# Kernel optimization log

Hardware: AMD Instinct MI355X
Metric: run time of the kernel (lower is better)

## Reference

```python
import jax, jax.numpy as jnp
import numpy as np

D_MODEL = 768
N_LAYER = 4
VOCAB = 50257
D_STATE = 16
D_CONV = 4
D_INNER = 2 * D_MODEL
DT_RANK = 48
B, L = 1, 2048


def setup_inputs() -> dict:
    key = jax.random.key(0)
    ks = jax.random.split(key, 12)
    n = lambda k, shape, s=0.02: jax.random.normal(k, shape, dtype=jnp.float32) * s
    return {
        "idx": jax.random.randint(ks[0], (B, L), 0, VOCAB, dtype=jnp.int32),
        "targets": jax.random.randint(ks[1], (B, L), 0, VOCAB, dtype=jnp.int32),
        "embedding": n(ks[2], (VOCAB, D_MODEL)),
        "norm_w": jnp.ones((N_LAYER, D_MODEL), jnp.float32),
        "in_proj_w": n(ks[3], (N_LAYER, 2 * D_INNER, D_MODEL)),
        "conv_w": n(ks[4], (N_LAYER, D_INNER, D_CONV), 0.1),
        "conv_b": jnp.zeros((N_LAYER, D_INNER), jnp.float32),
        "x_proj_w": n(ks[5], (N_LAYER, DT_RANK + 2 * D_STATE, D_INNER)),
        "dt_proj_w": n(ks[6], (N_LAYER, D_INNER, DT_RANK), 0.1),
        # bias so softplus(dt) lands in ~[0.01, 0.1] as in the official init
        "dt_proj_b": jax.random.uniform(ks[7], (N_LAYER, D_INNER), jnp.float32, -4.6, -2.3),
        # A_log = log(1..d_state), the standard S4D-real init
        "A_log": jnp.log(jnp.broadcast_to(jnp.arange(1, D_STATE + 1, dtype=jnp.float32), (N_LAYER, D_INNER, D_STATE))),
        "D_param": jnp.ones((N_LAYER, D_INNER), jnp.float32),
        "out_proj_w": n(ks[8], (N_LAYER, D_MODEL, D_INNER)),
        "norm_f_w": jnp.ones((D_MODEL,), jnp.float32),
    }


def rmsnorm(x, w, eps=1e-5):
    return x * jax.lax.rsqrt(jnp.mean(x * x, -1, keepdims=True) + eps) * w


def causal_conv1d(x, w, b):
    # x: (B,L,d_inner); w: (d_inner, K) depthwise causal conv
    K = w.shape[-1]
    Lx = x.shape[1]
    xp = jnp.pad(x, ((0, 0), (K - 1, 0), (0, 0)))
    y = b
    for k in range(K):
        y = y + xp[:, k:k + Lx, :] * w[:, k]
    return y


def selective_scan(x, dt, A, Bm, Cm, Dp):
    # x, dt: (B,L,d_inner); A: (d_inner,d_state); Bm, Cm: (B,L,d_state)
    bsz, _, d_in = x.shape

    def step(h, inp):
        x_t, dt_t, B_t, C_t = inp  # (B,d_in),(B,d_in),(B,s),(B,s)
        h = jnp.exp(dt_t[:, :, None] * A) * h + (dt_t * x_t)[:, :, None] * B_t[:, None, :]
        return h, jnp.einsum('bds,bs->bd', h, C_t)

    h0 = jnp.zeros((bsz, d_in, A.shape[-1]), x.dtype)
    _, ys = jax.lax.scan(step, h0, (x.swapaxes(0, 1), dt.swapaxes(0, 1), Bm.swapaxes(0, 1), Cm.swapaxes(0, 1)))
    return ys.swapaxes(0, 1) + x * Dp


def mamba_block(x, in_w, cw, cb, xpw, dtw, dtb, a_log, dp, ow):
    xz = x @ in_w.T  # (B,L,2*d_inner)
    xi, z = jnp.split(xz, 2, axis=-1)
    xi = jax.nn.silu(causal_conv1d(xi, cw, cb))
    xdbl = xi @ xpw.T  # (B,L,dt_rank+2*d_state)
    dt = xdbl[..., :DT_RANK]
    Bm = xdbl[..., DT_RANK:DT_RANK + D_STATE]
    Cm = xdbl[..., DT_RANK + D_STATE:]
    dt = jax.nn.softplus(dt @ dtw.T + dtb)
    A = -jnp.exp(a_log)
    y = selective_scan(xi, dt, A, Bm, Cm, dp)
    y = y * jax.nn.silu(z)
    return y @ ow.T


def reference(idx, targets, embedding, norm_w, in_proj_w, conv_w, conv_b, x_proj_w,
              dt_proj_w, dt_proj_b, A_log, D_param, out_proj_w, norm_f_w):
    x = embedding[idx]  # (B,L,D)
    for l in range(N_LAYER):
        x = x + mamba_block(rmsnorm(x, norm_w[l]), in_proj_w[l], conv_w[l], conv_b[l],
                            x_proj_w[l], dt_proj_w[l], dt_proj_b[l], A_log[l],
                            D_param[l], out_proj_w[l])
    x = rmsnorm(x, norm_f_w)
    logits = x @ embedding.T  # tied lm head, (B,L,V)
    # cross_entropy with ignore_index=-1
    logp = jax.nn.log_softmax(logits, axis=-1)
    mask = (targets >= 0).astype(logits.dtype)
    tgt = jnp.clip(targets, 0, VOCAB - 1)
    nll = -jnp.take_along_axis(logp, tgt[..., None], axis=-1)[..., 0]
    loss = jnp.sum(nll * mask) / jnp.maximum(jnp.sum(mask), 1.0)
    return (logits, loss)
```

## Files before the change

### kernel.cpp

```cpp
#include <hip/hip_runtime.h>
#include <stdint.h>


#define D_MODEL 768
#define N_LAYER 4
#define VOCAB 50257
#define D_STATE 16
#define D_INNER 1536
#define DT_RANK 48
#define LSEQ 2048
#define TCHUNK 64
#define NCHUNK 32

#define EMB_E 39321600L
#define W1E 2359296L
#define W2E 196608L
#define W3E 98304L
#define W4E 1179648L
#define PERL (W1E + W2E + W3E + W4E)
#define TOTCVT (EMB_E + 4 * PERL)

typedef unsigned short u16;
typedef __attribute__((ext_vector_type(8))) short short8;
typedef __attribute__((ext_vector_type(4))) float f32x4;

__device__ __forceinline__ u16 f2bf(float f) {
  unsigned int x = __float_as_uint(f);
  x += 0x7fffu + ((x >> 16) & 1u);
  return (u16)(x >> 16);
}
__device__ __forceinline__ float bf2f(u16 v) {
  return __uint_as_float(((unsigned int)v) << 16);
}
__device__ __forceinline__ void gl16(const void* g, void* l) {
  __builtin_amdgcn_global_load_lds((const __attribute__((address_space(1))) void*)g,
                                   (__attribute__((address_space(3))) void*)l, 16, 0, 0);
}

#define PIPELINE(NT)                                                          \
  STAGE(0, 0);                                                                \
  STAGE(32, 1);                                                               \
  {                                                                           \
    int cur = 0;                                                              \
    for (int t = 0; t < (NT); t++) {                                          \
      if (t + 1 < (NT)) { asm volatile("s_waitcnt vmcnt(4)" ::: "memory"); }  \
      else              { asm volatile("s_waitcnt vmcnt(0)" ::: "memory"); }  \
      asm volatile("s_barrier" ::: "memory");                                 \
      short8 af[4], bfr[4];                                                   \
      _Pragma("unroll")                                                       \
      for (int i = 0; i < 4; i++)                                             \
        af[i] = *(const short8*)(&lA[cur][(wm + i * 16 + fr) * 32 + kh]);     \
      _Pragma("unroll")                                                       \
      for (int j = 0; j < 4; j++)                                             \
        bfr[j] = *(const short8*)(&lB[cur][(wn + j * 16 + fr) * 32 + kh]);    \
      asm volatile("s_waitcnt lgkmcnt(0)" ::: "memory");                      \
      asm volatile("s_barrier" ::: "memory");                                 \
      if (t + 2 < (NT)) STAGE((t + 2) * 32, cur);                             \
      _Pragma("unroll")                                                       \
      for (int i = 0; i < 4; i++)                                             \
        _Pragma("unroll")                                                     \
        for (int j = 0; j < 4; j++)                                           \
          acc[i][j] = __builtin_amdgcn_mfma_f32_16x16x32_bf16(af[i], bfr[j],  \
                                                              acc[i][j], 0, 0, 0); \
      cur ^= 1;                                                               \
    }                                                                         \
  }

__global__ void k_convert_all(const float* __restrict__ emb, const float* __restrict__ in_w,
                              const float* __restrict__ xp_w, const float* __restrict__ dt_w,
                              const float* __restrict__ out_w, u16* __restrict__ dst) {
  long i = (long)blockIdx.x * 256 + threadIdx.x;
  float v;
  if (i < EMB_E) {
    long n = i / D_MODEL, k = i % D_MODEL;
    v = (n < VOCAB) ? emb[n * D_MODEL + k] : 0.0f;
  } else {
    long j = i - EMB_E;
    int l = (int)(j / PERL);
    long m = j % PERL;
    if (m < W1E) {
      v = in_w[(long)l * W1E + m];
    } else if (m < W1E + W2E) {
      long mm = m - W1E;
      long n = mm / D_INNER, k = mm % D_INNER;
      v = (n < 80) ? xp_w[(long)l * 80 * D_INNER + n * D_INNER + k] : 0.0f;
    } else if (m < W1E + W2E + W3E) {
      long mm = m - (W1E + W2E);
      long n = mm / 64, k = mm % 64;
      v = (k < DT_RANK) ? dt_w[(long)l * D_INNER * DT_RANK + n * DT_RANK + k] : 0.0f;
    } else {
      long mm = m - (W1E + W2E + W3E);
      v = out_w[(long)l * W4E + mm];
    }
  }
  dst[i] = f2bf(v);
}

__global__ void k_embed_rms(const int* __restrict__ idx, const float* __restrict__ emb,
                            const float* __restrict__ w, float* __restrict__ x,
                            u16* __restrict__ xnb) {
  int t = blockIdx.x, tid = threadIdx.x;
  __shared__ float red[256];
  const float* src = emb + (long)idx[t] * D_MODEL;
  float g[3];
  float s = 0.0f;
#pragma unroll
  for (int q = 0; q < 3; q++) {
    g[q] = src[tid + q * 256];
    s += g[q] * g[q];
  }
  red[tid] = s; __syncthreads();
  for (int o = 128; o > 0; o >>= 1) { if (tid < o) red[tid] += red[tid + o]; __syncthreads(); }
  float scale = rsqrtf(red[0] / (float)D_MODEL + 1e-5f);
#pragma unroll
  for (int q = 0; q < 3; q++) {
    int c = tid + q * 256;
    x[(long)t * D_MODEL + c] = g[q];
    xnb[(long)t * D_MODEL + c] = f2bf(g[q] * scale * w[c]);
  }
}

__global__ void k_rms_red(const float* __restrict__ part, const float* __restrict__ w,
                          float* __restrict__ x, u16* __restrict__ xnb) {
  int t = blockIdx.x, tid = threadIdx.x;
  __shared__ float red[256];
  float g[3];
  float s = 0.0f;
#pragma unroll
  for (int q = 0; q < 3; q++) {
    int c = tid + q * 256;
    long off = (long)t * D_MODEL + c;
    float v = x[off];
#pragma unroll
    for (int p = 0; p < 4; p++) v += part[(size_t)p * LSEQ * D_MODEL + off];
    g[q] = v;
    s += v * v;
  }
  red[tid] = s; __syncthreads();
  for (int o = 128; o > 0; o >>= 1) { if (tid < o) red[tid] += red[tid + o]; __syncthreads(); }
  float scale = rsqrtf(red[0] / (float)D_MODEL + 1e-5f);
#pragma unroll
  for (int q = 0; q < 3; q++) {
    int c = tid + q * 256;
    x[(long)t * D_MODEL + c] = g[q];
    xnb[(long)t * D_MODEL + c] = f2bf(g[q] * scale * w[c]);
  }
}

template<int EPI>
__global__ __launch_bounds__(256) void k_gemm2(
    const u16* __restrict__ A, const u16* __restrict__ W, void* __restrict__ Cv,
    const float* __restrict__ bias, int N, int K, int lda, int ldb, int ldc) {
  __shared__ u16 lA[2][128 * 32];
  __shared__ u16 lB[2][128 * 32];
  const int gx = gridDim.x, gy = gridDim.y;
  int id = blockIdx.x + gx * blockIdx.y;
  int q8 = (gx * gy) >> 3;
  int v = (id & 7) * q8 + (id >> 3);
  const int bx = v / gy, by = v % gy;
  const int brow = by * 128, bcol = bx * 128;
  const int tid = threadIdx.x, wid = tid >> 6, lane = tid & 63;
  const int wm = (wid >> 1) * 64, wn = (wid & 1) * 64;
  const int fr = lane & 15, fq = lane >> 4, kh = fq * 8;
  const int srow = tid >> 2, scol = (tid & 3) * 8;
  const u16* ga0 = A + (size_t)(brow + srow) * lda + scol;
  const u16* ga1 = A + (size_t)(brow + srow + 64) * lda + scol;
  const u16* gb0 = W + (size_t)(bcol + srow) * ldb + scol;
  const u16* gb1 = W + (size_t)(bcol + srow + 64) * ldb + scol;
  const int lo = srow * 32 + scol;

  f32x4 acc[4][4];
#pragma unroll
  for (int i = 0; i < 4; i++)
#pragma unroll
    for (int j = 0; j < 4; j++)
#pragma unroll
      for (int r = 0; r < 4; r++) acc[i][j][r] = 0.0f;

  auto STAGE = [&](int k0, int b) {
    gl16(ga0 + k0, &lA[b][lo]);
    gl16(ga1 + k0, &lA[b][lo + 2048]);
    gl16(gb0 + k0, &lB[b][lo]);
    gl16(gb1 + k0, &lB[b][lo + 2048]);
  };

  PIPELINE(K / 32);

#pragma unroll
  for (int i = 0; i < 4; i++)
#pragma unroll
    for (int j = 0; j < 4; j++) {
      int col = bcol + wn + j * 16 + fr;
      if (col < N) {
#pragma unroll
        for (int r = 0; r < 4; r++) {
          int row = brow + wm + i * 16 + fq * 4 + r;
          float val = acc[i][j][r];
          if (EPI == 1) {
            val += bias[col];
            val = (val > 20.0f) ? val : log1pf(__expf(val));
            ((float*)Cv)[(size_t)row * ldc + col] = val;
          } else {
            ((u16*)Cv)[(size_t)row * ldc + col] = f2bf(val);
          }
        }
      }
    }
}

__global__ __launch_bounds__(256) void k_gemm_part(
    const u16* __restrict__ A, const u16* __restrict__ W, float* __restrict__ Cp,
    int N, int Ks, int lda, int ldb, int ldc) {
  __shared__ u16 lA[2][128 * 32];
  __shared__ u16 lB[2][128 * 32];
  const int gx = gridDim.x, gy = gridDim.y;
  int id = blockIdx.x + gx * blockIdx.y;
  int q8 = (gx * gy) >> 3;
  int v = (id & 7) * q8 + (id >> 3);
  const int bx = v / gy, by = v % gy;
  const int brow = by * 128, bcol = bx * 128;
  const int koff = blockIdx.z * Ks;
  const int tid = threadIdx.x, wid = tid >> 6, lane = tid & 63;
  const int wm = (wid >> 1) * 64, wn = (wid & 1) * 64;
  const int fr = lane & 15, fq = lane >> 4, kh = fq * 8;
  const int srow = tid >> 2, scol = (tid & 3) * 8;
  const u16* ga0 = A + (size_t)(brow + srow) * lda + koff + scol;
  const u16* ga1 = A + (size_t)(brow + srow + 64) * lda + koff + scol;
  const u16* gb0 = W + (size_t)(bcol + srow) * ldb + koff + scol;
  const u16* gb1 = W + (size_t)(bcol + srow + 64) * ldb + koff + scol;
  const int lo = srow * 32 + scol;

  f32x4 acc[4][4];
#pragma unroll
  for (int i = 0; i < 4; i++)
#pragma unroll
    for (int j = 0; j < 4; j++)
#pragma unroll
      for (int r = 0; r < 4; r++) acc[i][j][r] = 0.0f;

  auto STAGE = [&](int k0, int b) {
    gl16(ga0 + k0, &lA[b][lo]);
    gl16(ga1 + k0, &lA[b][lo + 2048]);
    gl16(gb0 + k0, &lB[b][lo]);
    gl16(gb1 + k0, &lB[b][lo + 2048]);
  };

  PIPELINE(Ks / 32);

  float* Cz = Cp + (size_t)blockIdx.z * LSEQ * ldc;
#pragma unroll
  for (int i = 0; i < 4; i++)
#pragma unroll
    for (int j = 0; j < 4; j++) {
      int col = bcol + wn + j * 16 + fr;
      if (col < N) {
#pragma unroll
        for (int r = 0; r < 4; r++) {
          int row = brow + wm + i * 16 + fq * 4 + r;
          Cz[(size_t)row * ldc + col] = acc[i][j][r];
        }
      }
    }
}

__global__ __launch_bounds__(256) void k_gemm_logits(
    const u16* __restrict__ A, const u16* __restrict__ W, float* __restrict__ C,
    float* __restrict__ part) {
  __shared__ u16 lA[2][128 * 32];
  __shared__ u16 lB[2][128 * 32];
  const int b = blockIdx.x;
  const int xcd = b & 7, slot = b >> 3;
  const int ct = xcd * 50 + (slot >> 4), rt = slot & 15;
  const int brow = rt * 128, bcol = ct * 128;
  const int tid = threadIdx.x, wid = tid >> 6, lane = tid & 63;
  const int wm = (wid >> 1) * 64, wn = (wid & 1) * 64;
  const int fr = lane & 15, fq = lane >> 4, kh = fq * 8;
  const int srow = tid >> 2, scol = (tid & 3) * 8;
  const u16* ga0 = A + (size_t)(brow + srow) * D_MODEL + scol;
  const u16* ga1 = A + (size_t)(brow + srow + 64) * D_MODEL + scol;
  const u16* gb0 = W + (size_t)(bcol + srow) * D_MODEL + scol;
  const u16* gb1 = W + (size_t)(bcol + srow + 64) * D_MODEL + scol;
  const int lo = srow * 32 + scol;

  f32x4 acc[4][4];
#pragma unroll
  for (int i = 0; i < 4; i++)
#pragma unroll
    for (int j = 0; j < 4; j++)
#pragma unroll
      for (int r = 0; r < 4; r++) acc[i][j][r] = 0.0f;

  auto STAGE = [&](int k0, int bb) {
    gl16(ga0 + k0, &lA[bb][lo]);
    gl16(ga1 + k0, &lA[bb][lo + 2048]);
    gl16(gb0 + k0, &lB[bb][lo]);
    gl16(gb1 + k0, &lB[bb][lo + 2048]);
  };

  PIPELINE(D_MODEL / 32);

  float rs[16];
#pragma unroll
  for (int q = 0; q < 16; q++) rs[q] = 0.0f;
#pragma unroll
  for (int i = 0; i < 4; i++)
#pragma unroll
    for (int j = 0; j < 4; j++) {
      int col = bcol + wn + j * 16 + fr;
      if (col < VOCAB) {
#pragma unroll
        for (int r = 0; r < 4; r++) {
          int row = brow + wm + i * 16 + fq * 4 + r;
          float val = acc[i][j][r];
          C[(size_t)row * VOCAB + col] = val;
          rs[i * 4 + r] += __expf(val - 20.0f);
        }
      }
    }
#pragma unroll
  for (int q = 0; q < 16; q++) {
    float s = rs[q];
    s += __shfl_xor(s, 1); s += __shfl_xor(s, 2);
    s += __shfl_xor(s, 4); s += __shfl_xor(s, 8);
    rs[q] = s;
  }
  if (fr == 0) {
    int pc = ct * 2 + (wn >> 6);
#pragma unroll
    for (int i = 0; i < 4; i++)
#pragma unroll
      for (int r = 0; r < 4; r++) {
        int row = brow + wm + i * 16 + fq * 4 + r;
        part[(size_t)pc * LSEQ + row] = rs[i * 4 + r];
      }
  }
}

__global__ void k_conv_silu(const u16* __restrict__ xzb, const float* __restrict__ cw,
                            const float* __restrict__ cb, u16* __restrict__ xib) {
  int i = blockIdx.x * 256 + threadIdx.x;
  int t = i / (D_INNER / 8), d8 = (i % (D_INNER / 8)) * 8;
  float acc[8];
#pragma unroll
  for (int q = 0; q < 8; q++) acc[q] = cb[d8 + q];
#pragma unroll
  for (int k = 0; k < 4; k++) {
    int tt = t - 3 + k;
    if (tt >= 0) {
      short8 v = *(const short8*)(xzb + (long)tt * (2 * D_INNER) + d8);
#pragma unroll
      for (int q = 0; q < 8; q++) acc[q] += bf2f((u16)v[q]) * cw[(d8 + q) * 4 + k];
    }
  }
  short8 o;
#pragma unroll
  for (int q = 0; q < 8; q++) {
    float s = acc[q] / (1.0f + __expf(-acc[q]));
    o[q] = (short)f2bf(s);
  }
  *(short8*)(xib + (long)t * D_INNER + d8) = o;
}

__global__ void k_red_xd(const float* __restrict__ pxp, float* __restrict__ xdbl,
                         u16* __restrict__ dtp) {
  int i = blockIdx.x * 256 + threadIdx.x;
  int t = i >> 7, k = i & 127;
  if (k < 80) {
    float s = 0.0f;
#pragma unroll
    for (int p = 0; p < 8; p++) s += pxp[(size_t)p * LSEQ * 80 + (long)t * 80 + k];
    xdbl[(long)t * 80 + k] = s;
    if (k < DT_RANK) dtp[(long)t * 64 + k] = f2bf(s);
    else if (k < 64) dtp[(long)t * 64 + k] = 0;
  }
}

__global__ void k_scanA(const float* __restrict__ dt, const u16* __restrict__ xi,
                        const float* __restrict__ xdbl, const float* __restrict__ a_log,
                        float* __restrict__ aprod, float* __restrict__ hend) {
  int d = blockIdx.x * 256 + threadIdx.x;
  int c = blockIdx.y;
  float A[16], ap[16], h[16];
#pragma unroll
  for (int s = 0; s < 16; s++) { A[s] = -__expf(a_log[d * 16 + s]); ap[s] = 1.0f; h[s] = 0.0f; }
  int t0 = c * TCHUNK;
  for (int t = t0; t < t0 + TCHUNK; t++) {
    float dtv = dt[(long)t * D_INNER + d], xv = bf2f(xi[(long)t * D_INNER + d]);
    float dx = dtv * xv;
    const float* Bp = xdbl + (long)t * 80 + DT_RANK;
#pragma unroll
    for (int s = 0; s < 16; s++) {
      float a = __expf(dtv * A[s]);
      h[s] = a * h[s] + dx * Bp[s];
      ap[s] *= a;
    }
  }
  long base = ((long)c * D_INNER + d) * 16;
#pragma unroll
  for (int s = 0; s < 16; s++) { aprod[base + s] = ap[s]; hend[base + s] = h[s]; }
}

__global__ void k_scanB(const float* __restrict__ aprod, const float* __restrict__ hend,
                        float* __restrict__ hinit) {
  int i = blockIdx.x * 256 + threadIdx.x;
  float h = 0.0f;
  for (int c = 0; c < NCHUNK; c++) {
    long idx = (long)c * D_INNER * 16 + i;
    hinit[idx] = h;
    h = aprod[idx] * h + hend[idx];
  }
}

__global__ void k_scanC(const float* __restrict__ dt, const u16* __restrict__ xi,
                        const float* __restrict__ xdbl, const float* __restrict__ a_log,
                        const float* __restrict__ hinit, const float* __restrict__ Dp,
                        const u16* __restrict__ xzb, u16* __restrict__ yb) {
  int d = blockIdx.x * 256 + threadIdx.x;
  int c = blockIdx.y;
  float A[16], h[16];
  long hb = (long)c * D_INNER * 16 + (long)d * 16;
#pragma unroll
  for (int s = 0; s < 16; s++) { A[s] = -__expf(a_log[d * 16 + s]); h[s] = hinit[hb + s]; }
  float Dv = Dp[d];
  int t0 = c * TCHUNK;
  for (int t = t0; t < t0 + TCHUNK; t++) {
    float dtv = dt[(long)t * D_INNER + d], xv = bf2f(xi[(long)t * D_INNER + d]);
    float dx = dtv * xv;
    const float* Bp = xdbl + (long)t * 80 + DT_RANK;
    const float* Cp = Bp + D_STATE;
    float o = xv * Dv;
#pragma unroll
    for (int s = 0; s < 16; s++) {
      float a = __expf(dtv * A[s]);
      h[s] = a * h[s] + dx * Bp[s];
      o += h[s] * Cp[s];
    }
    float z = bf2f(xzb[(long)t * (2 * D_INNER) + D_INNER + d]);
    yb[(long)t * D_INNER + d] = f2bf(o * (z / (1.0f + __expf(-z))));
  }
}

__global__ void k_lse_final(const float* __restrict__ part, const float* __restrict__ logits,
                            const int* __restrict__ tgt, float* __restrict__ nll,
                            float* __restrict__ msk) {
  int t = blockIdx.x * 256 + threadIdx.x;
  float s = 0.0f;
  for (int p = 0; p < 800; p++) s += part[(size_t)p * LSEQ + t];
  float lse = 20.0f + __logf(s);
  int tg = tgt[t];
  float mk = tg >= 0 ? 1.0f : 0.0f;
  int tc = tg < 0 ? 0 : (tg > VOCAB - 1 ? VOCAB - 1 : tg);
  nll[t] = (lse - logits[(size_t)t * VOCAB + tc]) * mk;
  msk[t] = mk;
}

__global__ void k_loss(const float* __restrict__ nll, const float* __restrict__ msk,
                       float* __restrict__ out) {
  int tid = threadIdx.x;
  __shared__ float r1[256], r2[256];
  float a = 0.0f, b = 0.0f;
  for (int i = tid; i < LSEQ; i += 256) { a += nll[i]; b += msk[i]; }
  r1[tid] = a; r2[tid] = b; __syncthreads();
  for (int o = 128; o > 0; o >>= 1) {
    if (tid < o) { r1[tid] += r1[tid + o]; r2[tid] += r2[tid + o]; }
    __syncthreads();
  }
  if (tid == 0) out[0] = r1[0] / fmaxf(r2[0], 1.0f);
}

extern "C" void kernel_launch(void* const* d_in, const int* in_sizes, int n_in,
                              void* d_out, int out_size, void* d_ws, size_t ws_size,
                              hipStream_t stream) {
  const int*   idx    = (const int*)d_in[0];
  const int*   tgt    = (const int*)d_in[1];
  const float* emb    = (const float*)d_in[2];
  const float* norm_w = (const float*)d_in[3];
  const float* in_w   = (const float*)d_in[4];
  const float* conv_w = (const float*)d_in[5];
  const float* conv_b = (const float*)d_in[6];
  const float* xp_w   = (const float*)d_in[7];
  const float* dt_w   = (const float*)d_in[8];
  const float* dt_b   = (const float*)d_in[9];
  const float* a_log  = (const float*)d_in[10];
  const float* d_par  = (const float*)d_in[11];
  const float* out_w  = (const float*)d_in[12];
  const float* normf  = (const float*)d_in[13];

  float* logits = (float*)d_out;
  float* loss   = logits + (size_t)LSEQ * VOCAB;

  char* base = (char*)d_ws;
  size_t off = 0;
  auto alloc = [&](size_t bytes) -> char* {
    char* r = base + off;
    off = (off + bytes + 255) & ~(size_t)255;
    return r;
  };
  u16*   wcat = (u16*)  alloc((size_t)TOTCVT * 2);
  float* x    = (float*)alloc((size_t)LSEQ * D_MODEL * 4);
  u16*   xnb  = (u16*)  alloc((size_t)LSEQ * D_MODEL * 2);
  u16*   xzb  = (u16*)  alloc((size_t)LSEQ * 2 * D_INNER * 2);
  u16*   xib  = (u16*)  alloc((size_t)LSEQ * D_INNER * 2);
  float* xdbl = (float*)alloc((size_t)LSEQ * 80 * 4);
  u16*   dtp  = (u16*)  alloc((size_t)LSEQ * 64 * 2);
  float* dtl  = (float*)alloc((size_t)LSEQ * D_INNER * 4);
  u16*   yb   = (u16*)  alloc((size_t)LSEQ * D_INNER * 2);
  float* pxp  = (float*)alloc((size_t)8 * LSEQ * 80 * 4);
  float* pop  = (float*)alloc((size_t)4 * LSEQ * D_MODEL * 4);
  float* apr  = (float*)alloc((size_t)NCHUNK * D_INNER * 16 * 4);
  float* hen  = (float*)alloc((size_t)NCHUNK * D_INNER * 16 * 4);
  float* hin  = (float*)alloc((size_t)NCHUNK * D_INNER * 16 * 4);
  float* nll  = (float*)alloc((size_t)LSEQ * 4);
  float* msk  = (float*)alloc((size_t)LSEQ * 4);
  float* part = pop;
  (void)ws_size; (void)in_sizes; (void)n_in; (void)out_size;

  const u16* embb = wcat;

  k_convert_all<<<(unsigned)(TOTCVT / 256), 256, 0, stream>>>(emb, in_w, xp_w, dt_w, out_w, wcat);
  k_embed_rms<<<LSEQ, 256, 0, stream>>>(idx, emb, norm_w, x, xnb);

  for (int l = 0; l < N_LAYER; l++) {
    const u16* w1 = wcat + EMB_E + (long)l * PERL;
    const u16* w2 = w1 + W1E;
    const u16* w3 = w2 + W2E;
    const u16* w4 = w3 + W3E;

    k_gemm2<2><<<dim3(24, 16), 256, 0, stream>>>(
        xnb, w1, xzb, nullptr, 2 * D_INNER, D_MODEL, D_MODEL, D_MODEL, 2 * D_INNER);

    k_conv_silu<<<(LSEQ * D_INNER / 8) / 256, 256, 0, stream>>>(
        xzb, conv_w + (long)l * D_INNER * 4, conv_b + l * D_INNER, xib);

    k_gemm_part<<<dim3(1, 16, 8), 256, 0, stream>>>(
        xib, w2, pxp, 80, D_INNER / 8, D_INNER, D_INNER, 80);
    k_red_xd<<<(LSEQ * 128) / 256, 256, 0, stream>>>(pxp, xdbl, dtp);

    k_gemm2<1><<<dim3(12, 16), 256, 0, stream>>>(
        dtp, w3, dtl, dt_b + l * D_INNER, D_INNER, 64, 64, 64, D_INNER);

    const float* al = a_log + (long)l * D_INNER * D_STATE;
    k_scanA<<<dim3(D_INNER / 256, NCHUNK), 256, 0, stream>>>(dtl, xib, xdbl, al, apr, hen);
    k_scanB<<<(D_INNER * 16) / 256, 256, 0, stream>>>(apr, hen, hin);
    k_scanC<<<dim3(D_INNER / 256, NCHUNK), 256, 0, stream>>>(
        dtl, xib, xdbl, al, hin, d_par + l * D_INNER, xzb, yb);

    k_gemm_part<<<dim3(6, 16, 4), 256, 0, stream>>>(
        yb, w4, pop, D_MODEL, D_INNER / 4, D_INNER, D_INNER, D_MODEL);

    const float* wn = (l < N_LAYER - 1) ? (norm_w + (l + 1) * D_MODEL) : normf;
    k_rms_red<<<LSEQ, 256, 0, stream>>>(pop, wn, x, xnb);
  }

  k_gemm_logits<<<400 * 16, 256, 0, stream>>>(xnb, embb, logits, part);
  k_lse_final<<<LSEQ / 256, 256, 0, stream>>>(part, logits, tgt, nll, msk);
  k_loss<<<1, 256, 0, stream>>>(nll, msk, loss);
}
```

Measured before the change: 1.210 ms.

## XOR-swizzle GEMM LDS layout and enlarge logits tile to 256x128

Adds an XOR swizzle to the K-column position of global-to-LDS staging and to the matching fragment reads in all GEMM kernels, to cut LDS bank conflicts. The logits GEMM tile grows to 256 rows per block with 8x4 MFMA accumulators per wave, halving the grid and how often embedding tiles are reloaded. Its software pipeline is now written inline with explicit waitcnt, barriers and setprio. The cost is higher register pressure under launch_bounds(256,2) and fewer blocks to hide latency.

```diff
diff --git a/kernel.cpp b/kernel.cpp
--- a/kernel.cpp
+++ b/kernel.cpp
@@ -161,13 +161,16 @@
   const int brow = by * 128, bcol = bx * 128;
   const int tid = threadIdx.x, wid = tid >> 6, lane = tid & 63;
   const int wm = (wid >> 1) * 64, wn = (wid & 1) * 64;
-  const int fr = lane & 15, fq = lane >> 4, kh = fq * 8;
-  const int srow = tid >> 2, scol = (tid & 3) * 8;
+  const int fr = lane & 15, fq = lane >> 4;
+  const int kh = 8 * (fq ^ ((fr >> 1) & 3));
+  const int srow = tid >> 2;
+  const int lcol = (tid & 3) * 8;
+  const int scol = 8 * ((tid & 3) ^ ((srow >> 1) & 3));
   const u16* ga0 = A + (size_t)(brow + srow) * lda + scol;
   const u16* ga1 = A + (size_t)(brow + srow + 64) * lda + scol;
   const u16* gb0 = W + (size_t)(bcol + srow) * ldb + scol;
   const u16* gb1 = W + (size_t)(bcol + srow + 64) * ldb + scol;
-  const int lo = srow * 32 + scol;
+  const int lo = srow * 32 + lcol;
 
   f32x4 acc[4][4];
 #pragma unroll
@@ -222,13 +225,16 @@
   const int koff = blockIdx.z * Ks;
   const int tid = threadIdx.x, wid = tid >> 6, lane = tid & 63;
   const int wm = (wid >> 1) * 64, wn = (wid & 1) * 64;
-  const int fr = lane & 15, fq = lane >> 4, kh = fq * 8;
-  const int srow = tid >> 2, scol = (tid & 3) * 8;
+  const int fr = lane & 15, fq = lane >> 4;
+  const int kh = 8 * (fq ^ ((fr >> 1) & 3));
+  const int srow = tid >> 2;
+  const int lcol = (tid & 3) * 8;
+  const int scol = 8 * ((tid & 3) ^ ((srow >> 1) & 3));
   const u16* ga0 = A + (size_t)(brow + srow) * lda + koff + scol;
   const u16* ga1 = A + (size_t)(brow + srow + 64) * lda + koff + scol;
   const u16* gb0 = W + (size_t)(bcol + srow) * ldb + koff + scol;
   const u16* gb1 = W + (size_t)(bcol + srow + 64) * ldb + koff + scol;
-  const int lo = srow * 32 + scol;
+  const int lo = srow * 32 + lcol;
 
   f32x4 acc[4][4];
 #pragma unroll
@@ -263,47 +269,76 @@
     }
 }
 
-__global__ __launch_bounds__(256) void k_gemm_logits(
+__global__ __launch_bounds__(256, 2) void k_gemm_logits(
     const u16* __restrict__ A, const u16* __restrict__ W, float* __restrict__ C,
     float* __restrict__ part) {
-  __shared__ u16 lA[2][128 * 32];
+  __shared__ u16 lA[2][256 * 32];
   __shared__ u16 lB[2][128 * 32];
   const int b = blockIdx.x;
   const int xcd = b & 7, slot = b >> 3;
-  const int ct = xcd * 50 + (slot >> 4), rt = slot & 15;
-  const int brow = rt * 128, bcol = ct * 128;
+  const int ct = xcd * 50 + (slot >> 3), rt = slot & 7;
+  const int brow = rt * 256, bcol = ct * 128;
   const int tid = threadIdx.x, wid = tid >> 6, lane = tid & 63;
-  const int wm = (wid >> 1) * 64, wn = (wid & 1) * 64;
-  const int fr = lane & 15, fq = lane >> 4, kh = fq * 8;
-  const int srow = tid >> 2, scol = (tid & 3) * 8;
-  const u16* ga0 = A + (size_t)(brow + srow) * D_MODEL + scol;
-  const u16* ga1 = A + (size_t)(brow + srow + 64) * D_MODEL + scol;
-  const u16* gb0 = W + (size_t)(bcol + srow) * D_MODEL + scol;
-  const u16* gb1 = W + (size_t)(bcol + srow + 64) * D_MODEL + scol;
-  const int lo = srow * 32 + scol;
-
-  f32x4 acc[4][4];
-#pragma unroll
-  for (int i = 0; i < 4; i++)
+  const int wm = (wid >> 1) * 128, wn = (wid & 1) * 64;
+  const int fr = lane & 15, fq = lane >> 4;
+  const int kh = 8 * (fq ^ ((fr >> 1) & 3));
+  const int srow = tid >> 2;
+  const int lcol = (tid & 3) * 8;
+  const int scol = 8 * ((tid & 3) ^ ((srow >> 1) & 3));
+  const u16* ga = A + (size_t)(brow + srow) * D_MODEL + scol;
+  const u16* gb = W + (size_t)(bcol + srow) * D_MODEL + scol;
+  const int lo = srow * 32 + lcol;
+
+  f32x4 acc[8][4];
+#pragma unroll
+  for (int i = 0; i < 8; i++)
 #pragma unroll
     for (int j = 0; j < 4; j++)
 #pragma unroll
       for (int r = 0; r < 4; r++) acc[i][j][r] = 0.0f;
 
   auto STAGE = [&](int k0, int bb) {
-    gl16(ga0 + k0, &lA[bb][lo]);
-    gl16(ga1 + k0, &lA[bb][lo + 2048]);
-    gl16(gb0 + k0, &lB[bb][lo]);
-    gl16(gb1 + k0, &lB[bb][lo + 2048]);
+    gl16(ga + k0, &lA[bb][lo]);
+    gl16(ga + (size_t)64 * D_MODEL + k0, &lA[bb][lo + 2048]);
+    gl16(ga + (size_t)128 * D_MODEL + k0, &lA[bb][lo + 4096]);
+    gl16(ga + (size_t)192 * D_MODEL + k0, &lA[bb][lo + 6144]);
+    gl16(gb + k0, &lB[bb][lo]);
+    gl16(gb + (size_t)64 * D_MODEL + k0, &lB[bb][lo + 2048]);
   };
 
-  PIPELINE(D_MODEL / 32);
-
-  float rs[16];
-#pragma unroll
-  for (int q = 0; q < 16; q++) rs[q] = 0.0f;
-#pragma unroll
-  for (int i = 0; i < 4; i++)
+  STAGE(0, 0);
+  STAGE(32, 1);
+  int cur = 0;
+  const int NT = D_MODEL / 32;
+  for (int t = 0; t < NT; t++) {
+    if (t + 1 < NT) { asm volatile("s_waitcnt vmcnt(6)" ::: "memory"); }
+    else            { asm volatile("s_waitcnt vmcnt(0)" ::: "memory"); }
+    asm volatile("s_barrier" ::: "memory");
+    short8 af[8], bfr[4];
+#pragma unroll
+    for (int i = 0; i < 8; i++)
+      af[i] = *(const short8*)(&lA[cur][(wm + i * 16 + fr) * 32 + kh]);
+#pragma unroll
+    for (int j = 0; j < 4; j++)
+      bfr[j] = *(const short8*)(&lB[cur][(wn + j * 16 + fr) * 32 + kh]);
+    asm volatile("s_waitcnt lgkmcnt(0)" ::: "memory");
+    asm volatile("s_barrier" ::: "memory");
+    if (t + 2 < NT) STAGE((t + 2) * 32, cur);
+    __builtin_amdgcn_s_setprio(1);
+#pragma unroll
+    for (int i = 0; i < 8; i++)
+#pragma unroll
+      for (int j = 0; j < 4; j++)
+        acc[i][j] = __builtin_amdgcn_mfma_f32_16x16x32_bf16(af[i], bfr[j], acc[i][j], 0, 0, 0);
+    __builtin_amdgcn_s_setprio(0);
+    cur ^= 1;
+  }
+
+  float rs[32];
+#pragma unroll
+  for (int q = 0; q < 32; q++) rs[q] = 0.0f;
+#pragma unroll
+  for (int i = 0; i < 8; i++)
 #pragma unroll
     for (int j = 0; j < 4; j++) {
       int col = bcol + wn + j * 16 + fr;
@@ -318,7 +353,7 @@
       }
     }
 #pragma unroll
-  for (int q = 0; q < 16; q++) {
+  for (int q = 0; q < 32; q++) {
     float s = rs[q];
     s += __shfl_xor(s, 1); s += __shfl_xor(s, 2);
     s += __shfl_xor(s, 4); s += __shfl_xor(s, 8);
@@ -327,7 +362,7 @@
   if (fr == 0) {
     int pc = ct * 2 + (wn >> 6);
 #pragma unroll
-    for (int i = 0; i < 4; i++)
+    for (int i = 0; i < 8; i++)
 #pragma unroll
       for (int r = 0; r < 4; r++) {
         int row = brow + wm + i * 16 + fq * 4 + r;
@@ -552,7 +587,7 @@
     k_rms_red<<<LSEQ, 256, 0, stream>>>(pop, wn, x, xnb);
   }
 
-  k_gemm_logits<<<400 * 16, 256, 0, stream>>>(xnb, embb, logits, part);
+  k_gemm_logits<<<400 * 8, 256, 0, stream>>>(xnb, embb, logits, part);
   k_lse_final<<<LSEQ / 256, 256, 0, stream>>>(part, logits, tgt, nll, msk);
   k_loss<<<1, 256, 0, stream>>>(nll, msk, loss);
 }
```

New measurement: 1.171 ms. 1.03x faster.
